# Performance work log

Hardware: AMD Instinct MI355X
Metric: run time of the kernel (lower is better)

## Reference

```python
import jax, jax.numpy as jnp
import numpy as np
from jax import lax

B, IN_C, H, W = 2, 256, 80, 80
OUT_C = 256
INTER = IN_C // 16          # 16
C4 = IN_C // 4              # 64
K = 3
DIL = [7, 5, 2, 1]
PADS = [(K + (K - 1) * (d - 1)) // 2 for d in DIL]  # same-padding per module formula


def conv2d(x, w, b=None, pad=0, dil=1, groups=1):
    out = lax.conv_general_dilated(
        x, w, (1, 1), [(pad, pad), (pad, pad)], rhs_dilation=(dil, dil),
        dimension_numbers=('NCHW', 'OIHW', 'NCHW'), feature_group_count=groups)
    if b is not None:
        out = out + b[None, :, None, None]
    return out


def bnorm(x, g, b, eps=1e-3):
    # BatchNorm2d in training mode (fresh module): biased batch stats, eps=0.001
    m = x.mean((0, 2, 3), keepdims=True)
    v = x.var((0, 2, 3), keepdims=True)
    return (x - m) * lax.rsqrt(v + eps) * g[None, :, None, None] + b[None, :, None, None]


def gnorm(x, g, b, groups=4, eps=1e-5):
    Bb, C, Hh, Ww = x.shape
    xr = x.reshape(Bb, groups, C // groups, Hh, Ww)
    m = xr.mean((2, 3, 4), keepdims=True)
    v = xr.var((2, 3, 4), keepdims=True)
    xr = (xr - m) * lax.rsqrt(v + eps)
    return xr.reshape(Bb, C, Hh, Ww) * g[None, :, None, None] + b[None, :, None, None]


def setup_inputs() -> dict:
    keys = jax.random.split(jax.random.key(0), 40)

    def w_init(k, shape):
        fan = float(np.prod(shape[1:]))
        return jax.random.normal(k, shape, jnp.float32) / np.sqrt(fan)

    d = {}
    d['z'] = jax.random.normal(keys[0], (B, IN_C, H, W), jnp.float32)
    for i in range(4):  # depthwise dilated convs: (C4, 1, 3, 3)
        d[f'w_at{i}'] = w_init(keys[1 + 2 * i], (C4, 1, K, K))
        d[f'b_at{i}'] = jax.random.normal(keys[2 + 2 * i], (C4,), jnp.float32) * 0.02
    d['gn_w'] = 1.0 + 0.05 * jax.random.normal(keys[9], (IN_C,), jnp.float32)
    d['gn_b'] = 0.05 * jax.random.normal(keys[10], (IN_C,), jnp.float32)
    d['conv_w'] = w_init(keys[11], (IN_C, IN_C, 1, 1))
    d['conv_b'] = jax.random.normal(keys[12], (IN_C,), jnp.float32) * 0.02
    d['c5a_w'] = w_init(keys[13], (INTER, IN_C, 3, 3))
    d['bn5a_w'] = 1.0 + 0.05 * jax.random.normal(keys[14], (INTER,), jnp.float32)
    d['bn5a_b'] = 0.05 * jax.random.normal(keys[15], (INTER,), jnp.float32)
    d['c5c_w'] = w_init(keys[16], (INTER, IN_C, 3, 3))
    d['bn5c_w'] = 1.0 + 0.05 * jax.random.normal(keys[17], (INTER,), jnp.float32)
    d['bn5c_b'] = 0.05 * jax.random.normal(keys[18], (INTER,), jnp.float32)
    d['pq_w'] = w_init(keys[19], (INTER // 8, INTER, 1, 1))
    d['pq_b'] = jax.random.normal(keys[20], (INTER // 8,), jnp.float32) * 0.02
    d['pk_w'] = w_init(keys[21], (INTER // 8, INTER, 1, 1))
    d['pk_b'] = jax.random.normal(keys[22], (INTER // 8,), jnp.float32) * 0.02
    d['pv_w'] = w_init(keys[23], (INTER, INTER, 1, 1))
    d['pv_b'] = jax.random.normal(keys[24], (INTER,), jnp.float32) * 0.02
    d['pa_gamma'] = 0.5 * jnp.ones((1,), jnp.float32)  # nonzero so attn path is exercised
    d['ca_gamma'] = 0.5 * jnp.ones((1,), jnp.float32)
    d['c5b_w'] = w_init(keys[25], (INTER, INTER, 3, 3))
    d['bn5b_w'] = 1.0 + 0.05 * jax.random.normal(keys[26], (INTER,), jnp.float32)
    d['bn5b_b'] = 0.05 * jax.random.normal(keys[27], (INTER,), jnp.float32)
    d['c5d_w'] = w_init(keys[28], (INTER, INTER, 3, 3))
    d['bn5d_w'] = 1.0 + 0.05 * jax.random.normal(keys[29], (INTER,), jnp.float32)
    d['bn5d_b'] = 0.05 * jax.random.normal(keys[30], (INTER,), jnp.float32)
    d['c6_w'] = w_init(keys[31], (OUT_C, INTER, 1, 1))
    d['c6_b'] = jax.random.normal(keys[32], (OUT_C,), jnp.float32) * 0.02
    return d


def reference(z, w_at0, b_at0, w_at1, b_at1, w_at2, b_at2, w_at3, b_at3,
              gn_w, gn_b, conv_w, conv_b,
              c5a_w, bn5a_w, bn5a_b, c5c_w, bn5c_w, bn5c_b,
              pq_w, pq_b, pk_w, pk_b, pv_w, pv_b, pa_gamma, ca_gamma,
              c5b_w, bn5b_w, bn5b_b, c5d_w, bn5d_w, bn5d_b, c6_w, c6_b):
    parts = jnp.split(z, 4, axis=1)
    ws = [w_at0, w_at1, w_at2, w_at3]
    bs = [b_at0, b_at1, b_at2, b_at3]
    zs = [conv2d(parts[i], ws[i], bs[i], pad=PADS[i], dil=DIL[i], groups=C4)
          for i in range(4)]
    zc = jnp.concatenate(zs, axis=1)
    zc = jax.nn.gelu(conv2d(gnorm(zc, gn_w, gn_b), conv_w, conv_b), approximate=False)

    # --- DABlock ---
    feat1 = jax.nn.relu(bnorm(conv2d(zc, c5a_w, pad=1), bn5a_w, bn5a_b))
    Bb, C, Hh, Ww = feat1.shape
    N = Hh * Ww
    # PAM: full HWxHW attention
    q = conv2d(feat1, pq_w, pq_b).reshape(Bb, -1, N)   # (B, C//8, N)
    k = conv2d(feat1, pk_w, pk_b).reshape(Bb, -1, N)
    v = conv2d(feat1, pv_w, pv_b).reshape(Bb, C, N)
    energy = jnp.einsum('bcn,bcm->bnm', q, k)          # (B, N, N)
    att = jax.nn.softmax(energy, axis=-1)
    pa = jnp.einsum('bcm,bnm->bcn', v, att).reshape(Bb, C, Hh, Ww)
    pa = pa_gamma * pa + feat1
    pa_conv = jax.nn.relu(bnorm(conv2d(pa, c5b_w, pad=1), bn5b_w, bn5b_b))

    feat2 = jax.nn.relu(bnorm(conv2d(zc, c5c_w, pad=1), bn5c_w, bn5c_b))
    # CAM: CxC attention
    xf = feat2.reshape(Bb, C, N)
    e = jnp.einsum('bcn,bdn->bcd', xf, xf)             # (B, C, C)
    e = e.max(-1, keepdims=True) - e
    att_c = jax.nn.softmax(e, axis=-1)
    ca = jnp.einsum('bcd,bdn->bcn', att_c, xf).reshape(Bb, C, Hh, Ww)
    ca = ca_gamma * ca + feat2
    ca_conv = jax.nn.relu(bnorm(conv2d(ca, c5d_w, pad=1), bn5d_w, bn5d_b))

    # Dropout2d(p=0.05) is identity in eval mode
    out = jax.nn.relu(conv2d(pa_conv + ca_conv, c6_w, c6_b))
    return out
```

## Files before the change

kernel.cpp:

```cpp
#include <hip/hip_runtime.h>
#include <math.h>

#define HW 6400

typedef __attribute__((ext_vector_type(8))) short bf16x8;
typedef __attribute__((ext_vector_type(4))) float f32x4;

__device__ __forceinline__ float wredsum(float v){
  #pragma unroll
  for (int o = 32; o; o >>= 1) v += __shfl_xor(v, o);
  return v;
}

__device__ __forceinline__ unsigned short f2bf(float f){
  unsigned int u = __float_as_uint(f);
  u += 0x7FFF + ((u >> 16) & 1);
  return (unsigned short)(u >> 16);
}

__device__ __forceinline__ unsigned int cvt_pk_bf16(float lo, float hi){
  unsigned int r;
  asm("v_cvt_pk_bf16_f32 %0, %1, %2" : "=v"(r) : "v"(lo), "v"(hi));
  return r;
}

__device__ __forceinline__ float gelu(float v){
  return 0.5f * v * (1.f + erff(v * 0.70710678118f));
}

__global__ __launch_bounds__(256) void k_prep(
    const float* __restrict__ wa, const float* __restrict__ wc,
    const float* __restrict__ wb, const float* __restrict__ wd,
    const float* __restrict__ cw, const float* __restrict__ gn_sc,
    const float* __restrict__ cb,
    float* __restrict__ wt2, unsigned short* __restrict__ wbbf,
    unsigned short* __restrict__ cwbf, float* __restrict__ cbp){
  int bx = blockIdx.x;
  int tid = threadIdx.x;
  if (bx < 288){
    int i = bx * 256 + tid;
    if (i < 16 * 288){
      int ic = i / 288, r = i - ic * 288;
      int o = r / 9, k = r - o * 9;
      float v = (o < 16) ? wb[(o * 16 + ic) * 9 + k] : wd[((o - 16) * 16 + ic) * 9 + k];
      wt2[i] = v;
    }
    if (i < 73728){
      int j = i & 7, l = (i >> 3) & 63, f = (i >> 9) & 1, ss = i >> 10;
      int k = ss * 32 + (l >> 4) * 8 + j;
      int off = k >> 8, ic = k & 255;
      int oc = f * 16 + (l & 15);
      float v = (oc < 16) ? wa[(oc * 256 + ic) * 9 + off]
                          : wc[((oc - 16) * 256 + ic) * 9 + off];
      wbbf[i] = f2bf(v);
    }
  } else if (bx < 800){
    int i = (bx - 288) * 256 + tid;
    int b = i >> 16, r = i & 65535;
    int j = r & 7, l = (r >> 3) & 63, f = (r >> 9) & 15, ss = r >> 13;
    int ic = ss * 32 + (l >> 4) * 8 + j;
    int oc = f * 16 + (l & 15);
    cwbf[i] = f2bf(cw[oc * 256 + ic] * gn_sc[(b * 256 + ic) * 2]);
  } else {
    int bb = bx - 800;
    int b = bb >> 4;
    int oc = (bb & 15) * 16 + (tid >> 4);
    int cp = tid & 15;
    float s2 = 0.f;
    #pragma unroll
    for (int k = 0; k < 16; k++){
      int c = cp * 16 + k;
      s2 += cw[oc * 256 + c] * gn_sc[(b * 256 + c) * 2 + 1];
    }
    s2 += __shfl_xor(s2, 1); s2 += __shfl_xor(s2, 2);
    s2 += __shfl_xor(s2, 4); s2 += __shfl_xor(s2, 8);
    if (cp == 0) cbp[b * 256 + oc] = cb[oc] + s2;
  }
}

__global__ __launch_bounds__(256) void k_dwt(
    const float* __restrict__ z,
    const float* __restrict__ w0, const float* __restrict__ b0,
    const float* __restrict__ w1, const float* __restrict__ b1,
    const float* __restrict__ w2, const float* __restrict__ b2,
    const float* __restrict__ w3, const float* __restrict__ b3,
    unsigned short* __restrict__ zbf, float* __restrict__ gnpart){
  __shared__ unsigned short lt[64][66];
  int tid = threadIdx.x;
  int g = blockIdx.y, b = blockIdx.z;
  int p0 = blockIdx.x * 64;
  int lane = tid & 63, s = tid >> 6;
  int pix = p0 + lane;
  int h = pix / 80, w = pix % 80;
  const float* wp; const float* bp; int d;
  if (g == 0){ wp = w0; bp = b0; d = 7; }
  else if (g == 1){ wp = w1; bp = b1; d = 5; }
  else if (g == 2){ wp = w2; bp = b2; d = 2; }
  else            { wp = w3; bp = b3; d = 1; }
  int offr[9]; float msk[9];
  #pragma unroll
  for (int kh = 0; kh < 3; kh++){
    #pragma unroll
    for (int kw = 0; kw < 3; kw++){
      bool ok = ((unsigned)(h + (kh - 1) * d) < 80u) && ((unsigned)(w + (kw - 1) * d) < 80u);
      offr[kh * 3 + kw] = ok ? ((kh - 1) * d * 80 + (kw - 1) * d) : 0;
      msk[kh * 3 + kw] = ok ? 1.f : 0.f;
    }
  }
  const float* zb = z + (size_t)(b * 256 + g * 64) * HW + pix;
  for (int j = 0; j < 16; j++){
    int cl = s * 16 + j;
    const float* zin = zb + (size_t)cl * HW;
    const float* wr = wp + cl * 9;
    float acc = bp[cl];
    #pragma unroll
    for (int k = 0; k < 9; k++) acc = fmaf(wr[k], zin[offr[k]] * msk[k], acc);
    float S = wredsum(acc), Q = wredsum(acc * acc);
    if (lane == 0){
      int cg = b * 256 + g * 64 + cl;
      gnpart[(cg * 100 + blockIdx.x) * 2]     = S;
      gnpart[(cg * 100 + blockIdx.x) * 2 + 1] = Q;
    }
    lt[lane][cl] = f2bf(acc);
  }
  __syncthreads();
  int pr = tid >> 2, q = tid & 3;
  const unsigned short* src = &lt[pr][q * 16];
  unsigned int tmp[8];
  #pragma unroll
  for (int u = 0; u < 8; u++) tmp[u] = *(const unsigned int*)(src + u * 2);
  uint4 v0 = make_uint4(tmp[0], tmp[1], tmp[2], tmp[3]);
  uint4 v1 = make_uint4(tmp[4], tmp[5], tmp[6], tmp[7]);
  unsigned short* dst = zbf + ((size_t)b * HW + p0 + pr) * 256 + g * 64 + q * 16;
  *(uint4*)dst = v0;
  *(uint4*)(dst + 8) = v1;
}

__global__ __launch_bounds__(256) void k_gnfin(
    const float* __restrict__ gnpart, const float* __restrict__ gn_w,
    const float* __restrict__ gn_b, float* __restrict__ gn_sc){
  int tid = threadIdx.x; int bg = blockIdx.x;
  int b = bg >> 2, g = bg & 3;
  size_t base = (size_t)(b * 256 + g * 64) * 200;
  float S = 0.f, Q = 0.f;
  for (int i = tid; i < 6400; i += 256){
    S += gnpart[base + 2 * i];
    Q += gnpart[base + 2 * i + 1];
  }
  S = wredsum(S); Q = wredsum(Q);
  __shared__ float l[8];
  int lane = tid & 63, wid = tid >> 6;
  if (lane == 0){ l[wid] = S; l[4 + wid] = Q; }
  __syncthreads();
  float SS = l[0] + l[1] + l[2] + l[3];
  float QQ = l[4] + l[5] + l[6] + l[7];
  float M = 64.f * HW;
  float mean = SS / M;
  float var = QQ / M - mean * mean;
  float rstd = rsqrtf(var + 1e-5f);
  if (tid < 64){
    int c = g * 64 + tid;
    float sc = gn_w[c] * rstd;
    float sh = gn_b[c] - mean * sc;
    gn_sc[(b * 256 + c) * 2] = sc;
    gn_sc[(b * 256 + c) * 2 + 1] = sh;
  }
}

__global__ __launch_bounds__(256) void k_conv1_mfma(
    const unsigned short* __restrict__ zbf,
    const unsigned short* __restrict__ cwbf,
    const float* __restrict__ cbp,
    unsigned short* __restrict__ zbfT){
  __shared__ __align__(16) unsigned char lmem[64 * 512];
  unsigned short* lda = (unsigned short*)lmem;
  unsigned short* lout = (unsigned short*)lmem;
  int tid = threadIdx.x;
  int p0 = blockIdx.x * 64, ocg = blockIdx.y, b = blockIdx.z;
  #pragma unroll
  for (int k = 0; k < 8; k++){
    int m = tid + k * 256;
    int i = m >> 5, c = m & 31;
    bf16x8 val = *(const bf16x8*)(zbf + ((size_t)b * HW + p0 + i) * 256 + c * 8);
    *(bf16x8*)(lda + i * 256 + (c ^ (i & 7)) * 8) = val;
  }
  __syncthreads();
  int wv = tid >> 6, l = tid & 63;
  int row = l & 15, kg = l >> 4;
  int i = wv * 16 + row;
  f32x4 acc0 = {0.f,0.f,0.f,0.f}, acc1 = {0.f,0.f,0.f,0.f};
  f32x4 acc2 = {0.f,0.f,0.f,0.f}, acc3 = {0.f,0.f,0.f,0.f};
  const unsigned short* wp = cwbf + (size_t)b * 65536 + (ocg * 4) * 512 + l * 8;
  #pragma unroll
  for (int s = 0; s < 8; s++){
    int c = s * 4 + kg;
    bf16x8 a = *(const bf16x8*)(lda + i * 256 + (c ^ (i & 7)) * 8);
    const unsigned short* wps = wp + s * 8192;
    bf16x8 b0 = *(const bf16x8*)(wps);
    bf16x8 b1 = *(const bf16x8*)(wps + 512);
    bf16x8 b2 = *(const bf16x8*)(wps + 1024);
    bf16x8 b3 = *(const bf16x8*)(wps + 1536);
    acc0 = __builtin_amdgcn_mfma_f32_16x16x32_bf16(a, b0, acc0, 0, 0, 0);
    acc1 = __builtin_amdgcn_mfma_f32_16x16x32_bf16(a, b1, acc1, 0, 0, 0);
    acc2 = __builtin_amdgcn_mfma_f32_16x16x32_bf16(a, b2, acc2, 0, 0, 0);
    acc3 = __builtin_amdgcn_mfma_f32_16x16x32_bf16(a, b3, acc3, 0, 0, 0);
  }
  __syncthreads();
  const float* cbb = cbp + b * 256 + ocg * 64;
  int oc_l = l & 15;
  int pl = wv * 16 + kg * 4;
  float bs0 = cbb[oc_l], bs1 = cbb[16 + oc_l], bs2 = cbb[32 + oc_l], bs3 = cbb[48 + oc_l];
  #pragma unroll
  for (int r = 0; r < 4; r++){
    lout[(pl + r) * 72 + oc_l]      = f2bf(gelu(acc0[r] + bs0));
    lout[(pl + r) * 72 + 16 + oc_l] = f2bf(gelu(acc1[r] + bs1));
    lout[(pl + r) * 72 + 32 + oc_l] = f2bf(gelu(acc2[r] + bs2));
    lout[(pl + r) * 72 + 48 + oc_l] = f2bf(gelu(acc3[r] + bs3));
  }
  __syncthreads();
  int pix = tid >> 2, q = tid & 3;
  unsigned short* dst = zbfT + ((size_t)b * HW + p0 + pix) * 256 + ocg * 64 + q * 16;
  const unsigned short* src = lout + pix * 72 + q * 16;
  *(uint4*)dst       = *(const uint4*)src;
  *(uint4*)(dst + 8) = *(const uint4*)(src + 8);
}

__device__ __forceinline__ void c5_gload(bf16x8* r, const unsigned short* zbase,
    int p0, int irow, int c31, const int* hh, const int* ww, int off){
  int dy = off / 3 - 1, dx = off % 3 - 1;
  int doff = dy * 80 + dx;
  #pragma unroll
  for (int k = 0; k < 8; k++){
    int op = p0 + irow + k * 8;
    bool v = ((unsigned)(hh[k] + dy) < 80u) && ((unsigned)(ww[k] + dx) < 80u);
    int sp = v ? (op + doff) : op;
    bf16x8 val = *(const bf16x8*)(zbase + (size_t)sp * 256 + c31 * 8);
    if (!v) val = (bf16x8){0, 0, 0, 0, 0, 0, 0, 0};
    r[k] = val;
  }
}

__global__ __launch_bounds__(256) void k_conv5ac2(
    const unsigned short* __restrict__ zbfT,
    const unsigned short* __restrict__ wbbf,
    float* __restrict__ fpre, float* __restrict__ bnpart){
  __shared__ __align__(16) unsigned short lda[2][64 * 256];
  int tid = threadIdx.x;
  int och = blockIdx.y, b = blockIdx.z;
  int p0 = blockIdx.x * 64;
  int irow = tid >> 5, c31 = tid & 31;
  int hh[8], ww[8];
  #pragma unroll
  for (int k = 0; k < 8; k++){
    int op = p0 + irow + k * 8;
    hh[k] = op / 80; ww[k] = op % 80;
  }
  const unsigned short* zbase = zbfT + (size_t)b * HW * 256;
  bf16x8 r[8];
  c5_gload(r, zbase, p0, irow, c31, hh, ww, 0);
  #pragma unroll
  for (int k = 0; k < 8; k++){
    int i = irow + k * 8;
    *(bf16x8*)(lda[0] + i * 256 + (c31 ^ (i & 7)) * 8) = r[k];
  }
  c5_gload(r, zbase, p0, irow, c31, hh, ww, 1);
  int wv = tid >> 6, l = tid & 63;
  int lrow = l & 15, kg = l >> 4;
  int li = wv * 16 + lrow;
  f32x4 acc = {0.f, 0.f, 0.f, 0.f};
  for (int off = 0; off < 9; off++){
    __syncthreads();
    int buf = off & 1;
    const unsigned short* wp = wbbf + (size_t)off * 8192 + och * 512 + l * 8;
    #pragma unroll
    for (int s = 0; s < 8; s++){
      int cc = s * 4 + kg;
      bf16x8 a = *(const bf16x8*)(lda[buf] + li * 256 + (cc ^ (li & 7)) * 8);
      bf16x8 bb = *(const bf16x8*)(wp + s * 1024);
      acc = __builtin_amdgcn_mfma_f32_16x16x32_bf16(a, bb, acc, 0, 0, 0);
    }
    if (off + 1 < 9){
      #pragma unroll
      for (int k = 0; k < 8; k++){
        int i = irow + k * 8;
        *(bf16x8*)(lda[buf ^ 1] + i * 256 + (c31 ^ (i & 7)) * 8) = r[k];
      }
      if (off + 2 < 9) c5_gload(r, zbase, p0, irow, c31, hh, ww, off + 2);
    }
  }
  __syncthreads();
  float* lout = (float*)lda;
  int ocl = l & 15;
  int pl = wv * 16 + kg * 4;
  #pragma unroll
  for (int rr = 0; rr < 4; rr++) lout[ocl * 68 + pl + rr] = acc[rr];
  __syncthreads();
  int oc = tid >> 4, px = (tid & 15) * 4;
  float4 v = *(float4*)(lout + oc * 68 + px);
  *(float4*)(fpre + ((size_t)(b * 32 + och * 16 + oc)) * HW + p0 + px) = v;
  float S = v.x + v.y + v.z + v.w;
  float Q = v.x * v.x + v.y * v.y + v.z * v.z + v.w * v.w;
  #pragma unroll
  for (int o2 = 1; o2 < 16; o2 <<= 1){ S += __shfl_xor(S, o2); Q += __shfl_xor(Q, o2); }
  if ((tid & 15) == 0){
    int ocg = och * 16 + oc;
    bnpart[ocg * 400 + (b * 100 + blockIdx.x) * 2]     = S;
    bnpart[ocg * 400 + (b * 100 + blockIdx.x) * 2 + 1] = Q;
  }
}

__global__ __launch_bounds__(256) void k_featqkv(
    const float* __restrict__ fpre, const float* __restrict__ bnpart,
    const float* __restrict__ w1, const float* __restrict__ b1,
    const float* __restrict__ w2, const float* __restrict__ b2,
    const float* __restrict__ pqw, const float* __restrict__ pqb,
    const float* __restrict__ pkw, const float* __restrict__ pkb,
    const float* __restrict__ pvw, const float* __restrict__ pvb,
    float* __restrict__ feat, float* __restrict__ qkvT){
  __shared__ float lS[8][32], lQ[8][32], lsc[64];
  int tid = threadIdx.x; int b = blockIdx.y;
  {
    int oc = tid & 31, sl = tid >> 5;
    float S = 0.f, Q = 0.f;
    for (int i = sl; i < 200; i += 8){
      S += bnpart[oc * 400 + i * 2];
      Q += bnpart[oc * 400 + i * 2 + 1];
    }
    lS[sl][oc] = S; lQ[sl][oc] = Q;
    __syncthreads();
    if (tid < 32){
      float SS = 0.f, QQ = 0.f;
      #pragma unroll
      for (int s = 0; s < 8; s++){ SS += lS[s][tid]; QQ += lQ[s][tid]; }
      float M = 2.f * HW;
      float mean = SS / M, var = QQ / M - mean * mean;
      float rstd = rsqrtf(var + 1e-3f);
      float w  = (tid < 16) ? w1[tid] : w2[tid - 16];
      float bb = (tid < 16) ? b1[tid] : b2[tid - 16];
      float sc = w * rstd;
      lsc[tid * 2] = sc; lsc[tid * 2 + 1] = bb - mean * sc;
    }
    __syncthreads();
  }
  int n = blockIdx.x * 256 + tid;
  float f1[16], f2[16];
  #pragma unroll
  for (int c = 0; c < 16; c++){
    float v1 = fpre[(b * 32 + c) * HW + n] * lsc[c * 2] + lsc[c * 2 + 1];
    f1[c] = fmaxf(v1, 0.f);
    float v2 = fpre[(b * 32 + 16 + c) * HW + n] * lsc[(16 + c) * 2] + lsc[(16 + c) * 2 + 1];
    f2[c] = fmaxf(v2, 0.f);
    feat[(b * 32 + c) * HW + n] = f1[c];
    feat[(b * 32 + 16 + c) * HW + n] = f2[c];
  }
  float* o = qkvT + ((size_t)b * HW + n) * 20;
  #pragma unroll
  for (int j = 0; j < 2; j++){
    float q = pqb[j], k = pkb[j];
    #pragma unroll
    for (int c = 0; c < 16; c++){ q += pqw[j * 16 + c] * f1[c]; k += pkw[j * 16 + c] * f1[c]; }
    o[j] = q; o[2 + j] = k;
  }
  #pragma unroll
  for (int j = 0; j < 16; j++){
    float v = pvb[j];
    #pragma unroll
    for (int c = 0; c < 16; c++) v += pvw[j * 16 + c] * f1[c];
    o[4 + j] = v;
  }
}

__global__ __launch_bounds__(256) void k_pam_a(
    const float* __restrict__ qkvT, float* __restrict__ part){
  __shared__ __align__(16) float lk0[800];
  __shared__ __align__(16) float lk1[800];
  __shared__ __align__(16) unsigned short lvb[16][808];
  __shared__ float lred[4];
  int tid = threadIdx.x;
  int mc = blockIdx.y, b = blockIdx.z;
  float sqm = 0.f;
  for (int m = tid; m < 800; m += 256){
    const float* kv = qkvT + ((size_t)b * HW + mc * 800 + m) * 20;
    float4 a0 = *(const float4*)kv;
    lk0[m] = a0.z; lk1[m] = a0.w;
    sqm = fmaxf(sqm, a0.z * a0.z + a0.w * a0.w);
    float4 v0 = *(const float4*)(kv + 4);
    float4 v1 = *(const float4*)(kv + 8);
    float4 v2 = *(const float4*)(kv + 12);
    float4 v3 = *(const float4*)(kv + 16);
    lvb[0][m]  = f2bf(v0.x); lvb[1][m]  = f2bf(v0.y);
    lvb[2][m]  = f2bf(v0.z); lvb[3][m]  = f2bf(v0.w);
    lvb[4][m]  = f2bf(v1.x); lvb[5][m]  = f2bf(v1.y);
    lvb[6][m]  = f2bf(v1.z); lvb[7][m]  = f2bf(v1.w);
    lvb[8][m]  = f2bf(v2.x); lvb[9][m]  = f2bf(v2.y);
    lvb[10][m] = f2bf(v2.z); lvb[11][m] = f2bf(v2.w);
    lvb[12][m] = f2bf(v3.x); lvb[13][m] = f2bf(v3.y);
    lvb[14][m] = f2bf(v3.z); lvb[15][m] = f2bf(v3.w);
  }
  #pragma unroll
  for (int o = 32; o; o >>= 1) sqm = fmaxf(sqm, __shfl_xor(sqm, o));
  int lane = tid & 63, wid = tid >> 6;
  if (lane == 0) lred[wid] = sqm;
  __syncthreads();
  float kmax = sqrtf(fmaxf(fmaxf(lred[0], lred[1]), fmaxf(lred[2], lred[3])));
  int wv = tid >> 6, l = tid & 63;
  int row = l & 15, kg = l >> 4;
  int n = blockIdx.x * 64 + wv * 16 + row;
  const float* qp = qkvT + ((size_t)b * HW + n) * 20;
  float q0 = qp[0], q1 = qp[1];
  float mxr = sqrtf(q0 * q0 + q1 * q1) * kmax;
  f32x4 acc = {0.f, 0.f, 0.f, 0.f};
  float zp = 0.f;
  for (int t = 0; t < 25; t++){
    int m0 = t * 32 + kg * 8;
    float4 k0a = *(const float4*)&lk0[m0];
    float4 k0b = *(const float4*)&lk0[m0 + 4];
    float4 k1a = *(const float4*)&lk1[m0];
    float4 k1b = *(const float4*)&lk1[m0 + 4];
    float p0 = __expf(fmaf(q0, k0a.x, q1 * k1a.x) - mxr);
    float p1 = __expf(fmaf(q0, k0a.y, q1 * k1a.y) - mxr);
    float p2 = __expf(fmaf(q0, k0a.z, q1 * k1a.z) - mxr);
    float p3 = __expf(fmaf(q0, k0a.w, q1 * k1a.w) - mxr);
    float p4 = __expf(fmaf(q0, k0b.x, q1 * k1b.x) - mxr);
    float p5 = __expf(fmaf(q0, k0b.y, q1 * k1b.y) - mxr);
    float p6 = __expf(fmaf(q0, k0b.z, q1 * k1b.z) - mxr);
    float p7 = __expf(fmaf(q0, k0b.w, q1 * k1b.w) - mxr);
    zp += ((p0 + p1) + (p2 + p3)) + ((p4 + p5) + (p6 + p7));
    union { unsigned int u[4]; bf16x8 v; } pk;
    pk.u[0] = cvt_pk_bf16(p0, p1);
    pk.u[1] = cvt_pk_bf16(p2, p3);
    pk.u[2] = cvt_pk_bf16(p4, p5);
    pk.u[3] = cvt_pk_bf16(p6, p7);
    bf16x8 vb = *(const bf16x8*)&lvb[row][m0];
    acc = __builtin_amdgcn_mfma_f32_16x16x32_bf16(pk.v, vb, acc, 0, 0, 0);
  }
  zp += __shfl_xor(zp, 16);
  zp += __shfl_xor(zp, 32);
  float* pp = part + ((size_t)(b * 8 + mc) * 18) * HW;
  if (kg == 0){ pp[n] = mxr; pp[HW + n] = zp; }
  int c = l & 15;
  int nr = blockIdx.x * 64 + wv * 16 + (l >> 4) * 4;
  *(f32x4*)&pp[(size_t)(2 + c) * HW + nr] = acc;
}

__global__ __launch_bounds__(256) void k_cam_gram(
    const float* __restrict__ feat, float* __restrict__ e){
  int tid = threadIdx.x;
  int dd = blockIdx.x, c = blockIdx.y, b = blockIdx.z;
  const float* fc = feat + (b * 32 + 16 + c) * HW;
  const float* fd = feat + (b * 32 + 16 + dd) * HW;
  float S = 0.f;
  for (int i = tid; i < HW; i += 256) S += fc[i] * fd[i];
  S = wredsum(S);
  __shared__ float l[4];
  int lane = tid & 63, wid = tid >> 6;
  if (lane == 0) l[wid] = S;
  __syncthreads();
  if (tid == 0) e[(b * 16 + c) * 16 + dd] = l[0] + l[1] + l[2] + l[3];
}

__global__ __launch_bounds__(256) void k_merge(
    const float* __restrict__ part, const float* __restrict__ feat,
    const float* __restrict__ cam_e,
    const float* __restrict__ pa_g, const float* __restrict__ ca_g,
    float* __restrict__ pam_in, float* __restrict__ cam_in){
  int tid = threadIdx.x; int y = blockIdx.y, b = blockIdx.z;
  int n = blockIdx.x * 256 + tid;
  if (y < 8){
    int cg = y;
    float gamma = pa_g[0];
    float mxs[8]; float mx = -1e30f;
    #pragma unroll
    for (int mc = 0; mc < 8; mc++){
      mxs[mc] = part[((size_t)(b * 8 + mc) * 18) * HW + n];
      mx = fmaxf(mx, mxs[mc]);
    }
    float Z = 0.f, a0 = 0.f, a1 = 0.f;
    #pragma unroll
    for (int mc = 0; mc < 8; mc++){
      const float* pp = part + ((size_t)(b * 8 + mc) * 18) * HW + n;
      float r = __expf(mxs[mc] - mx);
      Z += pp[HW] * r;
      a0 += pp[(size_t)(2 + cg * 2) * HW] * r;
      a1 += pp[(size_t)(3 + cg * 2) * HW] * r;
    }
    float inv = gamma / Z;
    int c0 = cg * 2;
    pam_in[(b * 16 + c0) * HW + n]     = a0 * inv + feat[(b * 32 + c0) * HW + n];
    pam_in[(b * 16 + c0 + 1) * HW + n] = a1 * inv + feat[(b * 32 + c0 + 1) * HW + n];
  } else {
    int c = y - 8;
    const float* row = cam_e + (b * 16 + c) * 16;
    float r[16]; float mn = 1e30f;
    #pragma unroll
    for (int dd = 0; dd < 16; dd++){ r[dd] = row[dd]; mn = fminf(mn, r[dd]); }
    float p[16]; float ssum = 0.f;
    #pragma unroll
    for (int dd = 0; dd < 16; dd++){ p[dd] = __expf(mn - r[dd]); ssum += p[dd]; }
    float inv = ca_g[0] / ssum;
    float s = 0.f;
    #pragma unroll
    for (int dd = 0; dd < 16; dd++) s += p[dd] * feat[(b * 32 + 16 + dd) * HW + n];
    cam_in[(b * 16 + c) * HW + n] = s * inv + feat[(b * 32 + 16 + c) * HW + n];
  }
}

__global__ __launch_bounds__(64) void k_conv5bd2(
    const float* __restrict__ pam_in, const float* __restrict__ cam_in,
    const float* __restrict__ wt2,
    float* __restrict__ bdpre, float* __restrict__ bnpart){
  int tid = threadIdx.x;
  int pix = blockIdx.x * 64 + tid;
  int ocg = blockIdx.y, b = blockIdx.z;
  int half = ocg >> 2, oq = (ocg & 3) * 4;
  int h = pix / 80, w = pix % 80;
  int off[9]; float msk[9];
  #pragma unroll
  for (int dy = 0; dy < 3; dy++){
    #pragma unroll
    for (int dx = 0; dx < 3; dx++){
      int hh = h + dy - 1, ww = w + dx - 1;
      bool ok = ((unsigned)hh < 80u) && ((unsigned)ww < 80u);
      off[dy * 3 + dx] = ok ? hh * 80 + ww : 0;
      msk[dy * 3 + dx] = ok ? 1.f : 0.f;
    }
  }
  const float* in = (half ? cam_in : pam_in) + (size_t)b * 16 * HW;
  int obase = half * 16 + oq;
  float acc[4];
  #pragma unroll
  for (int o = 0; o < 4; o++) acc[o] = 0.f;
  float xa[9], xb[9];
  #pragma unroll
  for (int k = 0; k < 9; k++) xa[k] = in[off[k]] * msk[k];
  #pragma unroll
  for (int ic = 0; ic < 16; ic += 2){
    const float* xin1 = in + (size_t)(ic + 1) * HW;
    #pragma unroll
    for (int k = 0; k < 9; k++) xb[k] = xin1[off[k]] * msk[k];
    const float* wr0 = wt2 + ic * 288 + obase * 9;
    #pragma unroll
    for (int o = 0; o < 4; o++){
      float a = acc[o];
      #pragma unroll
      for (int k = 0; k < 9; k++) a += wr0[o * 9 + k] * xa[k];
      acc[o] = a;
    }
    if (ic + 2 < 16){
      const float* xin2 = in + (size_t)(ic + 2) * HW;
      #pragma unroll
      for (int k = 0; k < 9; k++) xa[k] = xin2[off[k]] * msk[k];
    }
    const float* wr1 = wt2 + (ic + 1) * 288 + obase * 9;
    #pragma unroll
    for (int o = 0; o < 4; o++){
      float a = acc[o];
      #pragma unroll
      for (int k = 0; k < 9; k++) a += wr1[o * 9 + k] * xb[k];
      acc[o] = a;
    }
  }
  #pragma unroll
  for (int o = 0; o < 4; o++){
    float v = acc[o];
    bdpre[(b * 32 + obase + o) * HW + pix] = v;
    float S = wredsum(v), Q = wredsum(v * v);
    if (tid == 0){
      bnpart[(obase + o) * 400 + (b * 100 + blockIdx.x) * 2]     = S;
      bnpart[(obase + o) * 400 + (b * 100 + blockIdx.x) * 2 + 1] = Q;
    }
  }
}

__global__ __launch_bounds__(256) void k_c6(
    const float* __restrict__ bdpre, const float* __restrict__ bnpart,
    const float* __restrict__ w1, const float* __restrict__ b1,
    const float* __restrict__ w2, const float* __restrict__ b2,
    const float* __restrict__ w6, const float* __restrict__ b6,
    float* __restrict__ out){
  __shared__ float lS[8][32], lQ[8][32], lsc[64];
  int tid = threadIdx.x; int og = blockIdx.y * 32, b = blockIdx.z;
  {
    int oc = tid & 31, sl = tid >> 5;
    float S = 0.f, Q = 0.f;
    for (int i = sl; i < 200; i += 8){
      S += bnpart[oc * 400 + i * 2];
      Q += bnpart[oc * 400 + i * 2 + 1];
    }
    lS[sl][oc] = S; lQ[sl][oc] = Q;
    __syncthreads();
    if (tid < 32){
      float SS = 0.f, QQ = 0.f;
      #pragma unroll
      for (int s = 0; s < 8; s++){ SS += lS[s][tid]; QQ += lQ[s][tid]; }
      float M = 2.f * HW;
      float mean = SS / M, var = QQ / M - mean * mean;
      float rstd = rsqrtf(var + 1e-3f);
      float w  = (tid < 16) ? w1[tid] : w2[tid - 16];
      float bb = (tid < 16) ? b1[tid] : b2[tid - 16];
      float sc = w * rstd;
      lsc[tid * 2] = sc; lsc[tid * 2 + 1] = bb - mean * sc;
    }
    __syncthreads();
  }
  int n = blockIdx.x * 256 + tid;
  float x[16];
  #pragma unroll
  for (int c = 0; c < 16; c++){
    float v1 = bdpre[(b * 32 + c) * HW + n] * lsc[c * 2] + lsc[c * 2 + 1];
    float v2 = bdpre[(b * 32 + 16 + c) * HW + n] * lsc[(16 + c) * 2] + lsc[(16 + c) * 2 + 1];
    x[c] = fmaxf(v1, 0.f) + fmaxf(v2, 0.f);
  }
  #pragma unroll
  for (int o = 0; o < 32; o++){
    float a = b6[og + o];
    #pragma unroll
    for (int c = 0; c < 16; c++) a += w6[(og + o) * 16 + c] * x[c];
    out[(b * 256 + og + o) * HW + n] = fmaxf(a, 0.f);
  }
}

extern "C" void kernel_launch(void* const* d_in, const int* in_sizes, int n_in,
                              void* d_out, int out_size, void* d_ws, size_t ws_size,
                              hipStream_t stream){
  const float* z      = (const float*)d_in[0];
  const float* w_at0  = (const float*)d_in[1];
  const float* b_at0  = (const float*)d_in[2];
  const float* w_at1  = (const float*)d_in[3];
  const float* b_at1  = (const float*)d_in[4];
  const float* w_at2  = (const float*)d_in[5];
  const float* b_at2  = (const float*)d_in[6];
  const float* w_at3  = (const float*)d_in[7];
  const float* b_at3  = (const float*)d_in[8];
  const float* gn_w   = (const float*)d_in[9];
  const float* gn_b   = (const float*)d_in[10];
  const float* conv_w = (const float*)d_in[11];
  const float* conv_b = (const float*)d_in[12];
  const float* c5a_w  = (const float*)d_in[13];
  const float* bn5a_w = (const float*)d_in[14];
  const float* bn5a_b = (const float*)d_in[15];
  const float* c5c_w  = (const float*)d_in[16];
  const float* bn5c_w = (const float*)d_in[17];
  const float* bn5c_b = (const float*)d_in[18];
  const float* pq_w   = (const float*)d_in[19];
  const float* pq_b   = (const float*)d_in[20];
  const float* pk_w   = (const float*)d_in[21];
  const float* pk_b   = (const float*)d_in[22];
  const float* pv_w   = (const float*)d_in[23];
  const float* pv_b   = (const float*)d_in[24];
  const float* pa_g   = (const float*)d_in[25];
  const float* ca_g   = (const float*)d_in[26];
  const float* c5b_w  = (const float*)d_in[27];
  const float* bn5b_w = (const float*)d_in[28];
  const float* bn5b_b = (const float*)d_in[29];
  const float* c5d_w  = (const float*)d_in[30];
  const float* bn5d_w = (const float*)d_in[31];
  const float* bn5d_b = (const float*)d_in[32];
  const float* c6_w   = (const float*)d_in[33];
  const float* c6_b   = (const float*)d_in[34];

  float* ws = (float*)d_ws;
  unsigned short* ZBF    = (unsigned short*)ws;
  unsigned short* ZC2BFT = (unsigned short*)(ws + 1638400);
  unsigned short* CWBF   = (unsigned short*)(ws + 3276800);
  float* CBP     = ws + 3407872;
  float* FPRE    = ws + 3408384;
  float* FEAT    = FPRE + 409600;
  float* QKVT    = FEAT + 409600;
  float* PAM_IN  = QKVT + 256000;
  float* CAM_IN  = PAM_IN + 204800;
  float* BDPRE   = CAM_IN + 204800;
  float* ST      = BDPRE + 409600;
  float* GN_SC    = ST;
  float* CAM_E    = ST + 1024;
  float* GN_PART  = ST + 2176;
  float* BNA_PART = ST + 104576;
  float* BNB_PART = ST + 117376;
  float* WT2      = ST + 130176;
  unsigned short* WBBF = (unsigned short*)(ST + 134784);
  float* PART = ws;

  k_dwt<<<dim3(100, 4, 2), 256, 0, stream>>>(z, w_at0, b_at0, w_at1, b_at1,
                                             w_at2, b_at2, w_at3, b_at3, ZBF, GN_PART);
  k_gnfin<<<8, 256, 0, stream>>>(GN_PART, gn_w, gn_b, GN_SC);
  k_prep<<<832, 256, 0, stream>>>(c5a_w, c5c_w, c5b_w, c5d_w, conv_w, GN_SC, conv_b,
                                  WT2, WBBF, CWBF, CBP);
  k_conv1_mfma<<<dim3(100, 4, 2), 256, 0, stream>>>(ZBF, CWBF, CBP, ZC2BFT);
  k_conv5ac2<<<dim3(100, 2, 2), 256, 0, stream>>>(ZC2BFT, WBBF, FPRE, BNA_PART);
  k_featqkv<<<dim3(25, 2), 256, 0, stream>>>(FPRE, BNA_PART, bn5a_w, bn5a_b,
                                             bn5c_w, bn5c_b, pq_w, pq_b, pk_w, pk_b,
                                             pv_w, pv_b, FEAT, QKVT);
  k_pam_a<<<dim3(100, 8, 2), 256, 0, stream>>>(QKVT, PART);
  k_cam_gram<<<dim3(16, 16, 2), 256, 0, stream>>>(FEAT, CAM_E);
  k_merge<<<dim3(25, 24, 2), 256, 0, stream>>>(PART, FEAT, CAM_E, pa_g, ca_g,
                                               PAM_IN, CAM_IN);
  k_conv5bd2<<<dim3(100, 8, 2), 64, 0, stream>>>(PAM_IN, CAM_IN, WT2, BDPRE, BNB_PART);
  k_c6<<<dim3(25, 8, 2), 256, 0, stream>>>(BDPRE, BNB_PART, bn5b_w, bn5b_b,
                                           bn5d_w, bn5d_b, c6_w, c6_b, (float*)d_out);
}
```

Before: 150.6 us.

## Move conv5b/5d to MFMA with bf16 pixel-major merge output

Replaces the scalar fp32 3x3 conv5b/conv5d kernel with an MFMA bf16 kernel. It uses block-diagonal packed weights, so both 16-channel convs run as one 32-wide K. The merge kernel is fused into one pass per pixel that writes PAM and CAM inputs as bf16 pixel-major rows, and the conv output is stored as bf16 for k_c6 to read. conv5ac2 also drops its double-buffered LDS in favour of a single buffer with an extra barrier. This gives up some precision through bf16 intermediates and lowers grid parallelism in merge and conv (25x2 and 100x2 blocks).

```diff
diff --git a/kernel.cpp b/kernel.cpp
--- a/kernel.cpp
+++ b/kernel.cpp
@@ -16,6 +16,10 @@
   unsigned int u = __float_as_uint(f);
   u += 0x7FFF + ((u >> 16) & 1);
   return (unsigned short)(u >> 16);
+}
+
+__device__ __forceinline__ float bf2f(unsigned short s){
+  return __uint_as_float((unsigned int)s << 16);
 }
 
 __device__ __forceinline__ unsigned int cvt_pk_bf16(float lo, float hi){
@@ -33,18 +37,13 @@
     const float* __restrict__ wb, const float* __restrict__ wd,
     const float* __restrict__ cw, const float* __restrict__ gn_sc,
     const float* __restrict__ cb,
-    float* __restrict__ wt2, unsigned short* __restrict__ wbbf,
-    unsigned short* __restrict__ cwbf, float* __restrict__ cbp){
+    unsigned short* __restrict__ wbbf,
+    unsigned short* __restrict__ cwbf, float* __restrict__ cbp,
+    unsigned short* __restrict__ wbbf2){
   int bx = blockIdx.x;
   int tid = threadIdx.x;
   if (bx < 288){
     int i = bx * 256 + tid;
-    if (i < 16 * 288){
-      int ic = i / 288, r = i - ic * 288;
-      int o = r / 9, k = r - o * 9;
-      float v = (o < 16) ? wb[(o * 16 + ic) * 9 + k] : wd[((o - 16) * 16 + ic) * 9 + k];
-      wt2[i] = v;
-    }
     if (i < 73728){
       int j = i & 7, l = (i >> 3) & 63, f = (i >> 9) & 1, ss = i >> 10;
       int k = ss * 32 + (l >> 4) * 8 + j;
@@ -61,7 +60,7 @@
     int ic = ss * 32 + (l >> 4) * 8 + j;
     int oc = f * 16 + (l & 15);
     cwbf[i] = f2bf(cw[oc * 256 + ic] * gn_sc[(b * 256 + ic) * 2]);
-  } else {
+  } else if (bx < 832){
     int bb = bx - 800;
     int b = bb >> 4;
     int oc = (bb & 15) * 16 + (tid >> 4);
@@ -75,6 +74,17 @@
     s2 += __shfl_xor(s2, 1); s2 += __shfl_xor(s2, 2);
     s2 += __shfl_xor(s2, 4); s2 += __shfl_xor(s2, 8);
     if (cp == 0) cbp[b * 256 + oc] = cb[oc] + s2;
+  } else {
+    int i = (bx - 832) * 256 + tid;
+    if (i < 9216){
+      int j = i & 7, l = (i >> 3) & 63, f = (i >> 9) & 1, off = i >> 10;
+      int kk = (l >> 4) * 8 + j;
+      int oc = f * 16 + (l & 15);
+      float v = 0.f;
+      if (oc < 16 && kk < 16)        v = wb[(oc * 16 + kk) * 9 + off];
+      else if (oc >= 16 && kk >= 16) v = wd[((oc - 16) * 16 + (kk - 16)) * 9 + off];
+      wbbf2[i] = f2bf(v);
+    }
   }
 }
 
@@ -244,7 +254,7 @@
     const unsigned short* __restrict__ zbfT,
     const unsigned short* __restrict__ wbbf,
     float* __restrict__ fpre, float* __restrict__ bnpart){
-  __shared__ __align__(16) unsigned short lda[2][64 * 256];
+  __shared__ __align__(16) unsigned short lda[64 * 256];
   int tid = threadIdx.x;
   int och = blockIdx.y, b = blockIdx.z;
   int p0 = blockIdx.x * 64;
@@ -261,7 +271,7 @@
   #pragma unroll
   for (int k = 0; k < 8; k++){
     int i = irow + k * 8;
-    *(bf16x8*)(lda[0] + i * 256 + (c31 ^ (i & 7)) * 8) = r[k];
+    *(bf16x8*)(lda + i * 256 + (c31 ^ (i & 7)) * 8) = r[k];
   }
   c5_gload(r, zbase, p0, irow, c31, hh, ww, 1);
   int wv = tid >> 6, l = tid & 63;
@@ -270,20 +280,20 @@
   f32x4 acc = {0.f, 0.f, 0.f, 0.f};
   for (int off = 0; off < 9; off++){
     __syncthreads();
-    int buf = off & 1;
     const unsigned short* wp = wbbf + (size_t)off * 8192 + och * 512 + l * 8;
     #pragma unroll
     for (int s = 0; s < 8; s++){
       int cc = s * 4 + kg;
-      bf16x8 a = *(const bf16x8*)(lda[buf] + li * 256 + (cc ^ (li & 7)) * 8);
+      bf16x8 a = *(const bf16x8*)(lda + li * 256 + (cc ^ (li & 7)) * 8);
       bf16x8 bb = *(const bf16x8*)(wp + s * 1024);
       acc = __builtin_amdgcn_mfma_f32_16x16x32_bf16(a, bb, acc, 0, 0, 0);
     }
     if (off + 1 < 9){
+      __syncthreads();
       #pragma unroll
       for (int k = 0; k < 8; k++){
         int i = irow + k * 8;
-        *(bf16x8*)(lda[buf ^ 1] + i * 256 + (c31 ^ (i & 7)) * 8) = r[k];
+        *(bf16x8*)(lda + i * 256 + (c31 ^ (i & 7)) * 8) = r[k];
       }
       if (off + 2 < 9) c5_gload(r, zbase, p0, irow, c31, hh, ww, off + 2);
     }
@@ -463,117 +473,145 @@
     const float* __restrict__ part, const float* __restrict__ feat,
     const float* __restrict__ cam_e,
     const float* __restrict__ pa_g, const float* __restrict__ ca_g,
-    float* __restrict__ pam_in, float* __restrict__ cam_in){
-  int tid = threadIdx.x; int y = blockIdx.y, b = blockIdx.z;
+    unsigned short* __restrict__ mc){
+  __shared__ float lsm[16][16];
+  int tid = threadIdx.x; int b = blockIdx.y;
+  if (tid < 16){
+    const float* rowe = cam_e + (b * 16 + tid) * 16;
+    float rr[16]; float mn = 1e30f;
+    #pragma unroll
+    for (int d = 0; d < 16; d++){ rr[d] = rowe[d]; mn = fminf(mn, rr[d]); }
+    float p[16]; float s = 0.f;
+    #pragma unroll
+    for (int d = 0; d < 16; d++){ p[d] = __expf(mn - rr[d]); s += p[d]; }
+    float inv = ca_g[0] / s;
+    #pragma unroll
+    for (int d = 0; d < 16; d++) lsm[tid][d] = p[d] * inv;
+  }
+  __syncthreads();
   int n = blockIdx.x * 256 + tid;
-  if (y < 8){
-    int cg = y;
-    float gamma = pa_g[0];
-    float mxs[8]; float mx = -1e30f;
-    #pragma unroll
-    for (int mc = 0; mc < 8; mc++){
-      mxs[mc] = part[((size_t)(b * 8 + mc) * 18) * HW + n];
-      mx = fmaxf(mx, mxs[mc]);
-    }
-    float Z = 0.f, a0 = 0.f, a1 = 0.f;
-    #pragma unroll
-    for (int mc = 0; mc < 8; mc++){
-      const float* pp = part + ((size_t)(b * 8 + mc) * 18) * HW + n;
-      float r = __expf(mxs[mc] - mx);
-      Z += pp[HW] * r;
-      a0 += pp[(size_t)(2 + cg * 2) * HW] * r;
-      a1 += pp[(size_t)(3 + cg * 2) * HW] * r;
-    }
-    float inv = gamma / Z;
-    int c0 = cg * 2;
-    pam_in[(b * 16 + c0) * HW + n]     = a0 * inv + feat[(b * 32 + c0) * HW + n];
-    pam_in[(b * 16 + c0 + 1) * HW + n] = a1 * inv + feat[(b * 32 + c0 + 1) * HW + n];
-  } else {
-    int c = y - 8;
-    const float* row = cam_e + (b * 16 + c) * 16;
-    float r[16]; float mn = 1e30f;
-    #pragma unroll
-    for (int dd = 0; dd < 16; dd++){ r[dd] = row[dd]; mn = fminf(mn, r[dd]); }
-    float p[16]; float ssum = 0.f;
-    #pragma unroll
-    for (int dd = 0; dd < 16; dd++){ p[dd] = __expf(mn - r[dd]); ssum += p[dd]; }
-    float inv = ca_g[0] / ssum;
+  float f1[16], f2[16];
+  #pragma unroll
+  for (int c = 0; c < 16; c++){
+    f1[c] = feat[(b * 32 + c) * HW + n];
+    f2[c] = feat[(b * 32 + 16 + c) * HW + n];
+  }
+  float mxs[8]; float mx = -1e30f;
+  #pragma unroll
+  for (int m8 = 0; m8 < 8; m8++){
+    mxs[m8] = part[((size_t)(b * 8 + m8) * 18) * HW + n];
+    mx = fmaxf(mx, mxs[m8]);
+  }
+  float Z = 0.f, a[16];
+  #pragma unroll
+  for (int c = 0; c < 16; c++) a[c] = 0.f;
+  #pragma unroll
+  for (int m8 = 0; m8 < 8; m8++){
+    const float* pp = part + ((size_t)(b * 8 + m8) * 18) * HW + n;
+    float r = __expf(mxs[m8] - mx);
+    Z += pp[HW] * r;
+    #pragma unroll
+    for (int c = 0; c < 16; c++) a[c] += pp[(size_t)(2 + c) * HW] * r;
+  }
+  float invp = pa_g[0] / Z;
+  union { unsigned short s[32]; uint4 u[4]; } rowo;
+  #pragma unroll
+  for (int c = 0; c < 16; c++)
+    rowo.s[c] = f2bf(fmaf(a[c], invp, f1[c]));
+  #pragma unroll
+  for (int c = 0; c < 16; c++){
     float s = 0.f;
     #pragma unroll
-    for (int dd = 0; dd < 16; dd++) s += p[dd] * feat[(b * 32 + 16 + dd) * HW + n];
-    cam_in[(b * 16 + c) * HW + n] = s * inv + feat[(b * 32 + 16 + c) * HW + n];
-  }
-}
-
-__global__ __launch_bounds__(64) void k_conv5bd2(
-    const float* __restrict__ pam_in, const float* __restrict__ cam_in,
-    const float* __restrict__ wt2,
-    float* __restrict__ bdpre, float* __restrict__ bnpart){
+    for (int d = 0; d < 16; d++) s = fmaf(lsm[c][d], f2[d], s);
+    rowo.s[16 + c] = f2bf(s + f2[c]);
+  }
+  unsigned short* dst = mc + ((size_t)b * HW + n) * 32;
+  *(uint4*)dst        = rowo.u[0];
+  *(uint4*)(dst + 8)  = rowo.u[1];
+  *(uint4*)(dst + 16) = rowo.u[2];
+  *(uint4*)(dst + 24) = rowo.u[3];
+}
+
+__global__ __launch_bounds__(256) void k_conv5bd_mfma(
+    const unsigned short* __restrict__ mc,
+    const unsigned short* __restrict__ wbbf2,
+    unsigned short* __restrict__ bdb, float* __restrict__ bnpart){
+  __shared__ __align__(16) unsigned short lda[9 * 2048];
+  __shared__ float lS[8][32], lQ[8][32];
   int tid = threadIdx.x;
-  int pix = blockIdx.x * 64 + tid;
-  int ocg = blockIdx.y, b = blockIdx.z;
-  int half = ocg >> 2, oq = (ocg & 3) * 4;
-  int h = pix / 80, w = pix % 80;
-  int off[9]; float msk[9];
-  #pragma unroll
-  for (int dy = 0; dy < 3; dy++){
-    #pragma unroll
-    for (int dx = 0; dx < 3; dx++){
-      int hh = h + dy - 1, ww = w + dx - 1;
-      bool ok = ((unsigned)hh < 80u) && ((unsigned)ww < 80u);
-      off[dy * 3 + dx] = ok ? hh * 80 + ww : 0;
-      msk[dy * 3 + dx] = ok ? 1.f : 0.f;
-    }
-  }
-  const float* in = (half ? cam_in : pam_in) + (size_t)b * 16 * HW;
-  int obase = half * 16 + oq;
-  float acc[4];
-  #pragma unroll
-  for (int o = 0; o < 4; o++) acc[o] = 0.f;
-  float xa[9], xb[9];
-  #pragma unroll
-  for (int k = 0; k < 9; k++) xa[k] = in[off[k]] * msk[k];
-  #pragma unroll
-  for (int ic = 0; ic < 16; ic += 2){
-    const float* xin1 = in + (size_t)(ic + 1) * HW;
-    #pragma unroll
-    for (int k = 0; k < 9; k++) xb[k] = xin1[off[k]] * msk[k];
-    const float* wr0 = wt2 + ic * 288 + obase * 9;
-    #pragma unroll
-    for (int o = 0; o < 4; o++){
-      float a = acc[o];
-      #pragma unroll
-      for (int k = 0; k < 9; k++) a += wr0[o * 9 + k] * xa[k];
-      acc[o] = a;
-    }
-    if (ic + 2 < 16){
-      const float* xin2 = in + (size_t)(ic + 2) * HW;
-      #pragma unroll
-      for (int k = 0; k < 9; k++) xa[k] = xin2[off[k]] * msk[k];
-    }
-    const float* wr1 = wt2 + (ic + 1) * 288 + obase * 9;
-    #pragma unroll
-    for (int o = 0; o < 4; o++){
-      float a = acc[o];
-      #pragma unroll
-      for (int k = 0; k < 9; k++) a += wr1[o * 9 + k] * xb[k];
-      acc[o] = a;
-    }
-  }
-  #pragma unroll
-  for (int o = 0; o < 4; o++){
-    float v = acc[o];
-    bdpre[(b * 32 + obase + o) * HW + pix] = v;
-    float S = wredsum(v), Q = wredsum(v * v);
-    if (tid == 0){
-      bnpart[(obase + o) * 400 + (b * 100 + blockIdx.x) * 2]     = S;
-      bnpart[(obase + o) * 400 + (b * 100 + blockIdx.x) * 2 + 1] = Q;
-    }
+  int b = blockIdx.z;
+  int p0 = blockIdx.x * 64;
+  int i = tid >> 2, q = tid & 3;
+  int op = p0 + i;
+  int h = op / 80, w = op % 80;
+  const unsigned short* mb = mc + (size_t)b * HW * 32;
+  #pragma unroll
+  for (int off = 0; off < 9; off++){
+    int dy = off / 3 - 1, dx = off % 3 - 1;
+    bool v = ((unsigned)(h + dy) < 80u) && ((unsigned)(w + dx) < 80u);
+    int sp = v ? (op + dy * 80 + dx) : op;
+    bf16x8 val = *(const bf16x8*)(mb + (size_t)sp * 32 + q * 8);
+    if (!v) val = (bf16x8){0, 0, 0, 0, 0, 0, 0, 0};
+    int c8 = ((i & 1) * 4 + q) ^ ((i >> 1) & 7);
+    *(bf16x8*)(lda + off * 2048 + (i >> 1) * 64 + c8 * 8) = val;
+  }
+  __syncthreads();
+  int wv = tid >> 6, l = tid & 63;
+  int row = l & 15, kg = l >> 4;
+  int i2 = wv * 16 + row;
+  f32x4 acc0 = {0.f, 0.f, 0.f, 0.f};
+  f32x4 acc1 = {0.f, 0.f, 0.f, 0.f};
+  #pragma unroll
+  for (int off = 0; off < 9; off++){
+    int c8 = ((i2 & 1) * 4 + kg) ^ ((i2 >> 1) & 7);
+    bf16x8 a = *(const bf16x8*)(lda + off * 2048 + (i2 >> 1) * 64 + c8 * 8);
+    bf16x8 b0 = *(const bf16x8*)(wbbf2 + off * 1024 + l * 8);
+    bf16x8 b1 = *(const bf16x8*)(wbbf2 + off * 1024 + 512 + l * 8);
+    acc0 = __builtin_amdgcn_mfma_f32_16x16x32_bf16(a, b0, acc0, 0, 0, 0);
+    acc1 = __builtin_amdgcn_mfma_f32_16x16x32_bf16(a, b1, acc1, 0, 0, 0);
+  }
+  __syncthreads();
+  float* lout = (float*)lda;
+  int ocl = l & 15;
+  int pl = wv * 16 + kg * 4;
+  #pragma unroll
+  for (int r = 0; r < 4; r++){
+    lout[(pl + r) * 34 + ocl]      = acc0[r];
+    lout[(pl + r) * 34 + 16 + ocl] = acc1[r];
+  }
+  __syncthreads();
+  {
+    int pix = tid >> 2, qq = tid & 3;
+    const float* src = lout + pix * 34 + qq * 8;
+    union { unsigned int u[4]; bf16x8 v; } pk;
+    pk.u[0] = cvt_pk_bf16(src[0], src[1]);
+    pk.u[1] = cvt_pk_bf16(src[2], src[3]);
+    pk.u[2] = cvt_pk_bf16(src[4], src[5]);
+    pk.u[3] = cvt_pk_bf16(src[6], src[7]);
+    *(bf16x8*)(bdb + ((size_t)b * HW + p0 + pix) * 32 + qq * 8) = pk.v;
+  }
+  {
+    int oc = tid & 31, grp = tid >> 5;
+    float S = 0.f, Q = 0.f;
+    #pragma unroll
+    for (int r = 0; r < 8; r++){
+      float v = lout[(grp * 8 + r) * 34 + oc];
+      S += v; Q += v * v;
+    }
+    lS[grp][oc] = S; lQ[grp][oc] = Q;
+  }
+  __syncthreads();
+  if (tid < 32){
+    float S = 0.f, Q = 0.f;
+    #pragma unroll
+    for (int g2 = 0; g2 < 8; g2++){ S += lS[g2][tid]; Q += lQ[g2][tid]; }
+    bnpart[tid * 400 + (b * 100 + blockIdx.x) * 2]     = S;
+    bnpart[tid * 400 + (b * 100 + blockIdx.x) * 2 + 1] = Q;
   }
 }
 
 __global__ __launch_bounds__(256) void k_c6(
-    const float* __restrict__ bdpre, const float* __restrict__ bnpart,
+    const unsigned short* __restrict__ bdb, const float* __restrict__ bnpart,
     const float* __restrict__ w1, const float* __restrict__ b1,
     const float* __restrict__ w2, const float* __restrict__ b2,
     const float* __restrict__ w6, const float* __restrict__ b6,
@@ -604,11 +642,17 @@
     __syncthreads();
   }
   int n = blockIdx.x * 256 + tid;
+  const unsigned short* rowp = bdb + ((size_t)b * HW + n) * 32;
+  union { bf16x8 v[4]; unsigned short s[32]; } r;
+  r.v[0] = *(const bf16x8*)(rowp);
+  r.v[1] = *(const bf16x8*)(rowp + 8);
+  r.v[2] = *(const bf16x8*)(rowp + 16);
+  r.v[3] = *(const bf16x8*)(rowp + 24);
   float x[16];
   #pragma unroll
   for (int c = 0; c < 16; c++){
-    float v1 = bdpre[(b * 32 + c) * HW + n] * lsc[c * 2] + lsc[c * 2 + 1];
-    float v2 = bdpre[(b * 32 + 16 + c) * HW + n] * lsc[(16 + c) * 2] + lsc[(16 + c) * 2 + 1];
+    float v1 = bf2f((unsigned short)r.s[c]) * lsc[c * 2] + lsc[c * 2 + 1];
+    float v2 = bf2f((unsigned short)r.s[16 + c]) * lsc[(16 + c) * 2] + lsc[(16 + c) * 2 + 1];
     x[c] = fmaxf(v1, 0.f) + fmaxf(v2, 0.f);
   }
   #pragma unroll
@@ -667,24 +711,23 @@
   float* FPRE    = ws + 3408384;
   float* FEAT    = FPRE + 409600;
   float* QKVT    = FEAT + 409600;
-  float* PAM_IN  = QKVT + 256000;
-  float* CAM_IN  = PAM_IN + 204800;
-  float* BDPRE   = CAM_IN + 204800;
-  float* ST      = BDPRE + 409600;
+  unsigned short* MC  = (unsigned short*)(QKVT + 256000);
+  unsigned short* BDB = (unsigned short*)(QKVT + 256000 + 204800);
+  float* ST      = QKVT + 256000 + 409600;
   float* GN_SC    = ST;
   float* CAM_E    = ST + 1024;
   float* GN_PART  = ST + 2176;
   float* BNA_PART = ST + 104576;
   float* BNB_PART = ST + 117376;
-  float* WT2      = ST + 130176;
-  unsigned short* WBBF = (unsigned short*)(ST + 134784);
+  unsigned short* WBBF  = (unsigned short*)(ST + 130176);
+  unsigned short* WBBF2 = (unsigned short*)(ST + 167040);
   float* PART = ws;
 
   k_dwt<<<dim3(100, 4, 2), 256, 0, stream>>>(z, w_at0, b_at0, w_at1, b_at1,
                                              w_at2, b_at2, w_at3, b_at3, ZBF, GN_PART);
   k_gnfin<<<8, 256, 0, stream>>>(GN_PART, gn_w, gn_b, GN_SC);
-  k_prep<<<832, 256, 0, stream>>>(c5a_w, c5c_w, c5b_w, c5d_w, conv_w, GN_SC, conv_b,
-                                  WT2, WBBF, CWBF, CBP);
+  k_prep<<<868, 256, 0, stream>>>(c5a_w, c5c_w, c5b_w, c5d_w, conv_w, GN_SC, conv_b,
+                                  WBBF, CWBF, CBP, WBBF2);
   k_conv1_mfma<<<dim3(100, 4, 2), 256, 0, stream>>>(ZBF, CWBF, CBP, ZC2BFT);
   k_conv5ac2<<<dim3(100, 2, 2), 256, 0, stream>>>(ZC2BFT, WBBF, FPRE, BNA_PART);
   k_featqkv<<<dim3(25, 2), 256, 0, stream>>>(FPRE, BNA_PART, bn5a_w, bn5a_b,
@@ -692,9 +735,8 @@
                                              pv_w, pv_b, FEAT, QKVT);
   k_pam_a<<<dim3(100, 8, 2), 256, 0, stream>>>(QKVT, PART);
   k_cam_gram<<<dim3(16, 16, 2), 256, 0, stream>>>(FEAT, CAM_E);
-  k_merge<<<dim3(25, 24, 2), 256, 0, stream>>>(PART, FEAT, CAM_E, pa_g, ca_g,
-                                               PAM_IN, CAM_IN);
-  k_conv5bd2<<<dim3(100, 8, 2), 64, 0, stream>>>(PAM_IN, CAM_IN, WT2, BDPRE, BNB_PART);
-  k_c6<<<dim3(25, 8, 2), 256, 0, stream>>>(BDPRE, BNB_PART, bn5b_w, bn5b_b,
+  k_merge<<<dim3(25, 2), 256, 0, stream>>>(PART, FEAT, CAM_E, pa_g, ca_g, MC);
+  k_conv5bd_mfma<<<dim3(100, 1, 2), 256, 0, stream>>>(MC, WBBF2, BDB, BNB_PART);
+  k_c6<<<dim3(25, 8, 2), 256, 0, stream>>>(BDB, BNB_PART, bn5b_w, bn5b_b,
                                            bn5d_w, bn5d_b, c6_w, c6_b, (float*)d_out);
 }
```

New measurement: 153.7 us. +2.1%, slower.
